# Optimization experiments

Measured on AMD Instinct MI355X. Metric: run time of the kernel, lower is better.

Reference implementation:

```python
import math
import jax, jax.numpy as jnp
import numpy as np

B, S, E, H = 2, 2048, 1024, 16
DK = E // H

def setup_inputs() -> dict:
    key = jax.random.key(0)
    ks = jax.random.split(key, 12)
    sc = 1.0 / math.sqrt(E)
    return {
        "x": jax.random.normal(ks[0], (B, S, E), jnp.float32),
        "kv": jax.random.normal(ks[1], (B, S, E), jnp.float32),
        "mask": jax.random.randint(ks[2], (B, S), 0, 2, jnp.int32),
        "attn_bias": jax.random.normal(ks[3], (B, S, S), jnp.float32),
        "WQ_w": jax.random.normal(ks[4], (E, E), jnp.float32) * sc,
        "WQ_b": jnp.zeros((E,), jnp.float32),
        "WK_w": jax.random.normal(ks[5], (E, E), jnp.float32) * sc,
        "WK_b": jnp.zeros((E,), jnp.float32),
        "WV_w": jax.random.normal(ks[6], (E, E), jnp.float32) * sc,
        "WV_b": jnp.zeros((E,), jnp.float32),
        "WO_w": jax.random.normal(ks[7], (E, E), jnp.float32) * sc,
        "WO_b": jnp.zeros((E,), jnp.float32),
    }

def reference(x, kv, mask, attn_bias, WQ_w, WQ_b, WK_w, WK_b, WV_w, WV_b, WO_w, WO_b):
    b, sq, _ = x.shape
    sk = kv.shape[1]
    # projections, split heads: [B,S,E] -> [B,H,S,DK]
    Q = (x @ WQ_w.T + WQ_b).reshape(b, sq, H, DK).transpose(0, 2, 1, 3)
    K = (kv @ WK_w.T + WK_b).reshape(b, sk, H, DK).transpose(0, 2, 1, 3)
    V = (kv @ WV_w.T + WV_b).reshape(b, sk, H, DK).transpose(0, 2, 1, 3)
    # scores [B,H,Sq,Sk]
    T = jnp.einsum('bhqd,bhkd->bhqk', Q, K) / math.sqrt(DK)
    T = T + attn_bias[:, None, :, :]  # 3D bias broadcast over heads
    m2 = jnp.einsum('bi,bj->bij', mask.astype(T.dtype), mask.astype(T.dtype))
    T = jnp.where(m2[:, None, :, :] == 0, jnp.asarray(-1e9, T.dtype), T)
    A = jax.nn.softmax(T, axis=-1)
    out = jnp.einsum('bhqk,bhkd->bhqd', A, V)  # [B,H,Sq,DK]
    out = out.transpose(0, 2, 1, 3).reshape(b, sq, E)
    return out @ WO_w.T + WO_b
```

## Files before the change

kernel.cpp:

```cpp
#include <hip/hip_runtime.h>

#define DEV static __device__ __forceinline__

typedef __attribute__((ext_vector_type(8))) __bf16 bf16x8;
typedef __attribute__((ext_vector_type(4))) float f32x4;

constexpr int CB = 2;
constexpr int CS = 2048;
constexpr int CE = 1024;
constexpr int CH = 16;
constexpr int CD = 64;
constexpr float LOG2E = 1.44269504f;

DEV unsigned short f2bf(float x) {
  unsigned int u = __float_as_uint(x);
  u += 0x7fffu + ((u >> 16) & 1u);
  return (unsigned short)(u >> 16);
}

DEV f32x4 mfma32(bf16x8 a, bf16x8 b, f32x4 c) {
  return __builtin_amdgcn_mfma_f32_16x16x32_bf16(a, b, c, 0, 0, 0);
}

DEV unsigned int cvtpk(float lo, float hi) {
  unsigned int r;
  asm("v_cvt_pk_bf16_f32 %0, %1, %2" : "=v"(r) : "v"(lo), "v"(hi));
  return r;
}

DEV float exp2r(float x) {
#if __has_builtin(__builtin_amdgcn_exp2f)
  return __builtin_amdgcn_exp2f(x);
#else
  float r; asm("v_exp_f32 %0, %1" : "=v"(r) : "v"(x)); return r;
#endif
}

DEV f32x4 unpk(unsigned int a, unsigned int b) {
  f32x4 r;
  r[0] = __uint_as_float(a << 16);
  r[1] = __uint_as_float(a & 0xffff0000u);
  r[2] = __uint_as_float(b << 16);
  r[3] = __uint_as_float(b & 0xffff0000u);
  return r;
}

DEV void stage16(const void* g, void* l) {
  __builtin_amdgcn_global_load_lds(
      (const __attribute__((address_space(1))) unsigned int*)g,
      (__attribute__((address_space(3))) unsigned int*)l, 16, 0, 0);
}

DEV void cvt_body(long i, const float* __restrict__ x, const float* __restrict__ kv,
                  const float* __restrict__ w0, const float* __restrict__ w1,
                  const float* __restrict__ w2, const float* __restrict__ w3,
                  unsigned short* __restrict__ out) {
  const long NE = (long)CB * CS * CE;
  const long WE = (long)CE * CE;
  const float* src;
  long off = i;
  if (i < NE) {
    src = x;
  } else if (i < 2 * NE) {
    src = kv; off = i - NE;
  } else {
    long j = i - 2 * NE;
    int wi = (int)(j >> 20);
    src = wi == 0 ? w0 : wi == 1 ? w1 : wi == 2 ? w2 : w3;
    off = j & (WE - 1);
  }
  float4 a = *reinterpret_cast<const float4*>(src + off);
  float4 b = *reinterpret_cast<const float4*>(src + off + 4);
  uint4 v;
  v.x = (unsigned int)f2bf(a.x) | ((unsigned int)f2bf(a.y) << 16);
  v.y = (unsigned int)f2bf(a.z) | ((unsigned int)f2bf(a.w) << 16);
  v.z = (unsigned int)f2bf(b.x) | ((unsigned int)f2bf(b.y) << 16);
  v.w = (unsigned int)f2bf(b.z) | ((unsigned int)f2bf(b.w) << 16);
  *reinterpret_cast<uint4*>(out + i) = v;
}

DEV void mbias_body(long idx, const float* __restrict__ bias, const int* __restrict__ mask,
                    unsigned short* __restrict__ mb16) {
  const int b = (int)(idx >> 22);
  const int q = (int)((idx >> 11) & (CS - 1));
  const int k0 = (int)(idx & (CS - 1));
  const bool mq = mask[b * CS + q] != 0;
  const int4 mk0 = *reinterpret_cast<const int4*>(mask + b * CS + k0);
  const int4 mk1 = *reinterpret_cast<const int4*>(mask + b * CS + k0 + 4);
  const float4 b0 = *reinterpret_cast<const float4*>(bias + idx);
  const float4 b1 = *reinterpret_cast<const float4*>(bias + idx + 4);
  const float NEG = -1e9f * LOG2E;
  float v[8];
  if (mq) {
    v[0] = (mk0.x != 0) ? b0.x * LOG2E : NEG;
    v[1] = (mk0.y != 0) ? b0.y * LOG2E : NEG;
    v[2] = (mk0.z != 0) ? b0.z * LOG2E : NEG;
    v[3] = (mk0.w != 0) ? b0.w * LOG2E : NEG;
    v[4] = (mk1.x != 0) ? b1.x * LOG2E : NEG;
    v[5] = (mk1.y != 0) ? b1.y * LOG2E : NEG;
    v[6] = (mk1.z != 0) ? b1.z * LOG2E : NEG;
    v[7] = (mk1.w != 0) ? b1.w * LOG2E : NEG;
  } else {
#pragma unroll
    for (int j = 0; j < 8; j++) v[j] = 0.f;
  }
  uint4 o;
  o.x = cvtpk(v[0], v[1]); o.y = cvtpk(v[2], v[3]);
  o.z = cvtpk(v[4], v[5]); o.w = cvtpk(v[6], v[7]);
  *reinterpret_cast<uint4*>(mb16 + idx) = o;
}

__global__ __launch_bounds__(256) void prep_all(const float* __restrict__ x,
                                                const float* __restrict__ kv,
                                                const float* __restrict__ w0,
                                                const float* __restrict__ w1,
                                                const float* __restrict__ w2,
                                                const float* __restrict__ w3,
                                                unsigned short* __restrict__ outcvt,
                                                const float* __restrict__ bias,
                                                const int* __restrict__ mask,
                                                unsigned short* __restrict__ mb16) {
  const long CVTB = (2 * (long)CB * CS * CE + 4 * (long)CE * CE) / 2048;
  if (blockIdx.x < CVTB) {
    cvt_body(((long)blockIdx.x * 256 + threadIdx.x) * 8, x, kv, w0, w1, w2, w3, outcvt);
  } else {
    mbias_body(((long)(blockIdx.x - CVTB) * 256 + threadIdx.x) * 8, bias, mask, mb16);
  }
}

__global__ __launch_bounds__(256) void cvt_all(const float* __restrict__ x,
                                               const float* __restrict__ kv,
                                               const float* __restrict__ w0,
                                               const float* __restrict__ w1,
                                               const float* __restrict__ w2,
                                               const float* __restrict__ w3,
                                               unsigned short* __restrict__ out) {
  cvt_body(((long)blockIdx.x * 256 + threadIdx.x) * 8, x, kv, w0, w1, w2, w3, out);
}
__global__ __launch_bounds__(256) void mk_mbias(const float* __restrict__ bias,
                                                const int* __restrict__ mask,
                                                unsigned short* __restrict__ mb16) {
  mbias_body(((long)blockIdx.x * 256 + threadIdx.x) * 8, bias, mask, mb16);
}

__global__ __launch_bounds__(256) void gemm_qkv(const unsigned short* __restrict__ xb,
                                                const unsigned short* __restrict__ kvb,
                                                const unsigned short* __restrict__ Wall,
                                                const float* __restrict__ bq,
                                                const float* __restrict__ bk,
                                                const float* __restrict__ bv,
                                                unsigned short* __restrict__ Qb) {
  __shared__ __align__(16) unsigned short As[128 * 64];
  __shared__ __align__(16) unsigned short Bs[128 * 64];
  const long NE = (long)CB * CS * CE;
  const long WE = (long)CE * CE;
  const int which = blockIdx.y >> 3;
  const int n0 = (blockIdx.y & 7) * 128;
  const unsigned short* A = which == 0 ? xb : kvb;
  const unsigned short* W = Wall + (long)which * WE;
  const float* bias = which == 0 ? bq : which == 1 ? bk : bv;
  const int tid = threadIdx.x;
  const int lane = tid & 63, wave = tid >> 6;
  const int wm = (wave >> 1) * 64, wn = (wave & 1) * 64;
  const int g = lane >> 4, rr = lane & 15;
  const int m0 = blockIdx.x * 128;
  const int K = CE;
  f32x4 acc[4][4] = {};

  for (int k0 = 0; k0 < K; k0 += 64) {
#pragma unroll
    for (int t = 0; t < 4; t++) {
      const int u = t * 256 + tid;
      const int row = u >> 3, ce = (u & 7) * 8;
      const int lb = (t * 256 + (tid & 192)) * 16;
      stage16(A + (long)(m0 + row) * K + k0 + ce, (char*)As + lb);
      stage16(W + (long)(n0 + row) * K + k0 + ce, (char*)Bs + lb);
    }
    __syncthreads();
#pragma unroll
    for (int kk = 0; kk < 2; kk++) {
      bf16x8 af[4], bfr[4];
#pragma unroll
      for (int i = 0; i < 4; i++)
        af[i] = *reinterpret_cast<const bf16x8*>(&As[(wm + i * 16 + rr) * 64 + kk * 32 + g * 8]);
#pragma unroll
      for (int j = 0; j < 4; j++)
        bfr[j] = *reinterpret_cast<const bf16x8*>(&Bs[(wn + j * 16 + rr) * 64 + kk * 32 + g * 8]);
#pragma unroll
      for (int i = 0; i < 4; i++)
#pragma unroll
        for (int j = 0; j < 4; j++)
          acc[i][j] = mfma32(af[i], bfr[j], acc[i][j]);
    }
    __syncthreads();
  }

  const float scale = which == 0 ? 0.125f * LOG2E : 1.0f;
#pragma unroll
  for (int i = 0; i < 4; i++) {
#pragma unroll
    for (int j = 0; j < 4; j++) {
      const int colg = n0 + wn + j * 16 + rr;
      const float bvv = bias[colg];
      if (which == 2) {
        const int rowbase = m0 + wm + i * 16 + g * 4;
        const int bb = rowbase >> 11, s = rowbase & 2047;
        const int hh = colg >> 6, d = colg & 63;
        uint2 val;
        val.x = (unsigned int)f2bf(acc[i][j][0] + bvv) | ((unsigned int)f2bf(acc[i][j][1] + bvv) << 16);
        val.y = (unsigned int)f2bf(acc[i][j][2] + bvv) | ((unsigned int)f2bf(acc[i][j][3] + bvv) << 16);
        *reinterpret_cast<uint2*>(Qb + 2 * NE + ((long)((bb * CH + hh) * CD + d)) * CS + s) = val;
      } else {
        unsigned short* outp = Qb + (long)which * NE;
#pragma unroll
        for (int r = 0; r < 4; r++) {
          const int row = m0 + wm + i * 16 + g * 4 + r;
          outp[(long)row * CE + colg] = f2bf((acc[i][j][r] + bvv) * scale);
        }
      }
    }
  }
}

__global__ __launch_bounds__(256) void gemm_wo(const unsigned short* __restrict__ A,
                                               const unsigned short* __restrict__ W,
                                               const float* __restrict__ bias,
                                               float* __restrict__ out) {
  __shared__ __align__(16) unsigned short As[128 * 64];
  __shared__ __align__(16) unsigned short Bs[64 * 64];
  const int tid = threadIdx.x;
  const int lane = tid & 63, wave = tid >> 6;
  const int wm = (wave >> 1) * 64, wn = (wave & 1) * 32;
  const int g = lane >> 4, rr = lane & 15;
  const int m0 = blockIdx.x * 128, n0 = blockIdx.y * 64;
  const int K = CE;
  f32x4 acc[4][2] = {};

  for (int k0 = 0; k0 < K; k0 += 64) {
#pragma unroll
    for (int t = 0; t < 4; t++) {
      const int u = t * 256 + tid;
      const int row = u >> 3, ce = (u & 7) * 8;
      stage16(A + (long)(m0 + row) * K + k0 + ce, (char*)As + (t * 256 + (tid & 192)) * 16);
    }
#pragma unroll
    for (int t = 0; t < 2; t++) {
      const int u = t * 256 + tid;
      const int row = u >> 3, ce = (u & 7) * 8;
      stage16(W + (long)(n0 + row) * K + k0 + ce, (char*)Bs + (t * 256 + (tid & 192)) * 16);
    }
    __syncthreads();
#pragma unroll
    for (int kk = 0; kk < 2; kk++) {
      bf16x8 af[4], bfr[2];
#pragma unroll
      for (int i = 0; i < 4; i++)
        af[i] = *reinterpret_cast<const bf16x8*>(&As[(wm + i * 16 + rr) * 64 + kk * 32 + g * 8]);
#pragma unroll
      for (int j = 0; j < 2; j++)
        bfr[j] = *reinterpret_cast<const bf16x8*>(&Bs[(wn + j * 16 + rr) * 64 + kk * 32 + g * 8]);
#pragma unroll
      for (int i = 0; i < 4; i++)
#pragma unroll
        for (int j = 0; j < 2; j++)
          acc[i][j] = mfma32(af[i], bfr[j], acc[i][j]);
    }
    __syncthreads();
  }

#pragma unroll
  for (int i = 0; i < 4; i++)
#pragma unroll
    for (int j = 0; j < 2; j++) {
      const int colg = n0 + wn + j * 16 + rr;
      const float bvv = bias[colg];
#pragma unroll
      for (int r = 0; r < 4; r++) {
        const int row = m0 + wm + i * 16 + g * 4 + r;
        out[(long)row * CE + colg] = acc[i][j][r] + bvv;
      }
    }
}

__global__ __launch_bounds__(256, 2) void attn_kernel(const unsigned short* __restrict__ Qb,
                                                      const unsigned short* __restrict__ Kb,
                                                      const unsigned short* __restrict__ Vtw,
                                                      const unsigned short* __restrict__ mb16,
                                                      const int* __restrict__ mask,
                                                      unsigned short* __restrict__ AO) {
  __shared__ __align__(16) unsigned char lds[65536];
  const int h = blockIdx.x, qt = blockIdx.y, b = blockIdx.z;
  const int tid = threadIdx.x;
  const int lane = tid & 63, w = tid >> 6;
  const int g = lane >> 4, c = lane & 15;
  const int qbase = qt * 128 + w * 32;

  bf16x8 qf[2][2];
#pragma unroll
  for (int qb = 0; qb < 2; qb++) {
    const unsigned short* Qrow = Qb + ((long)b * CS + qbase + qb * 16 + c) * CE + h * CD;
    qf[qb][0] = *reinterpret_cast<const bf16x8*>(Qrow + g * 8);
    qf[qb][1] = *reinterpret_cast<const bf16x8*>(Qrow + 32 + g * 8);
    if (mask[b * CS + qbase + qb * 16 + c] == 0) {
      qf[qb][0] = bf16x8{}; qf[qb][1] = bf16x8{};
    }
  }

  const unsigned char *kg[4], *vg[4];
  {
    const unsigned char* Ksrc = (const unsigned char*)(Kb + (long)b * CS * CE + h * CD);
    const unsigned char* Vsrc = (const unsigned char*)(Vtw + (long)(b * CH + h) * CD * CS);
    const int rr8 = lane >> 3;
    const int csw = ((lane & 7) << 4) ^ (rr8 << 4);
#pragma unroll
    for (int t = 0; t < 4; t++) {
      const int krow = t * 32 + w * 8 + rr8;
      const int key = (krow & 96) + ((krow >> 2) & 3) * 8 + ((krow >> 4) & 1) * 4 + (krow & 3);
      kg[t] = Ksrc + (long)key * (CE * 2) + csw;
      const int vrow = (t & 1) * 32 + w * 8 + rr8;
      vg[t] = Vsrc + (long)vrow * (CS * 2) + (t >> 1) * 128 + csw;
    }
  }
  const int sw = (c & 7) << 4;
  const unsigned char* rb0 = lds + c * 128 + ((g * 16) ^ sw);
  const unsigned char* rb1 = lds + c * 128 + ((64 + g * 16) ^ sw);

  const unsigned short* mbp0 = mb16 + ((long)b * CS + qbase + c) * CS + g * 8;
  const unsigned short* mbp1 = mb16 + ((long)b * CS + qbase + 16 + c) * CS + g * 8;

  f32x4 o[2][4] = {};
  f32x4 lsum4[2] = {};
  uint4 mbr[2][4];

  auto stage = [&](int bo) {
    unsigned char* kbuf = lds + bo;
    unsigned char* vbuf = lds + bo + 16384;
#pragma unroll
    for (int t = 0; t < 4; t++) {
      stage16(kg[t], kbuf + t * 4096 + w * 1024);
      stage16(vg[t], vbuf + (t >> 1) * 8192 + (t & 1) * 4096 + w * 1024);
      kg[t] += 128 * CE * 2;
      vg[t] += 128 * 2;
    }
  };
  auto load_mb = [&](bool adv) {
#pragma unroll
    for (int kb = 0; kb < 4; kb++) {
      mbr[0][kb] = *reinterpret_cast<const uint4*>(mbp0 + kb * 32);
      mbr[1][kb] = *reinterpret_cast<const uint4*>(mbp1 + kb * 32);
    }
    if (adv) { mbp0 += 128; mbp1 += 128; }
  };

  auto compute = [&](int bo, bool adv) {
    f32x4 sf[2][8];
    __builtin_amdgcn_s_setprio(1);
#pragma unroll
    for (int cb = 0; cb < 8; cb++) {
      const bf16x8 kf0 = *reinterpret_cast<const bf16x8*>(rb0 + bo + cb * 2048);
      const bf16x8 kf1 = *reinterpret_cast<const bf16x8*>(rb1 + bo + cb * 2048);
#pragma unroll
      for (int qb = 0; qb < 2; qb++) {
        const uint4 m = mbr[qb][cb >> 1];
        const f32x4 ci = (cb & 1) ? unpk(m.z, m.w) : unpk(m.x, m.y);
        f32x4 t = mfma32(kf0, qf[qb][0], ci);
        sf[qb][cb] = mfma32(kf1, qf[qb][1], t);
      }
    }
    __builtin_amdgcn_s_setprio(0);
    load_mb(adv);
    uint4 pw[2][4];
#pragma unroll
    for (int qb = 0; qb < 2; qb++)
#pragma unroll
      for (int kb = 0; kb < 4; kb++)
#pragma unroll
        for (int half = 0; half < 2; half++) {
          const int cb = 2 * kb + half;
          f32x4 pv;
          pv[0] = exp2r(sf[qb][cb][0]);
          pv[1] = exp2r(sf[qb][cb][1]);
          pv[2] = exp2r(sf[qb][cb][2]);
          pv[3] = exp2r(sf[qb][cb][3]);
          lsum4[qb] = lsum4[qb] + pv;
          if (half == 0) { pw[qb][kb].x = cvtpk(pv[0], pv[1]); pw[qb][kb].y = cvtpk(pv[2], pv[3]); }
          else           { pw[qb][kb].z = cvtpk(pv[0], pv[1]); pw[qb][kb].w = cvtpk(pv[2], pv[3]); }
        }
    __builtin_amdgcn_s_setprio(1);
#pragma unroll
    for (int nb = 0; nb < 4; nb++) {
#pragma unroll
      for (int kb = 0; kb < 4; kb++) {
        const unsigned char* rbx = (kb & 1) ? rb1 : rb0;
        const bf16x8 vf = *reinterpret_cast<const bf16x8*>(
            rbx + bo + 16384 + (kb >> 1) * 8192 + nb * 2048);
#pragma unroll
        for (int qb = 0; qb < 2; qb++)
          o[qb][nb] = mfma32(vf, __builtin_bit_cast(bf16x8, pw[qb][kb]), o[qb][nb]);
      }
    }
    __builtin_amdgcn_s_setprio(0);
  };

  stage(0);
  load_mb(true);
  stage(32768);

#pragma unroll 1
  for (int it = 0; it < 8; ++it) {
    asm volatile("s_waitcnt vmcnt(16)" ::: "memory");
    __builtin_amdgcn_s_barrier();
    __builtin_amdgcn_sched_barrier(0);
    compute(0, it < 7);
    __builtin_amdgcn_sched_barrier(0);
    __builtin_amdgcn_s_barrier();
    stage(0);
    asm volatile("s_waitcnt vmcnt(16)" ::: "memory");
    __builtin_amdgcn_s_barrier();
    __builtin_amdgcn_sched_barrier(0);
    compute(32768, it < 7);
    __builtin_amdgcn_sched_barrier(0);
    __builtin_amdgcn_s_barrier();
    stage(32768);
  }

#pragma unroll
  for (int qb = 0; qb < 2; qb++) {
    float lsum = (lsum4[qb][0] + lsum4[qb][1]) + (lsum4[qb][2] + lsum4[qb][3]);
    lsum += __shfl_xor(lsum, 16, 64);
    lsum += __shfl_xor(lsum, 32, 64);
    const float linv = 1.0f / lsum;
    unsigned short* Orow = AO + ((long)b * CS + qbase + qb * 16 + c) * CE + h * CD;
#pragma unroll
    for (int nb = 0; nb < 4; nb++) {
      uint2 val;
      val.x = (unsigned int)f2bf(o[qb][nb][0] * linv) | ((unsigned int)f2bf(o[qb][nb][1] * linv) << 16);
      val.y = (unsigned int)f2bf(o[qb][nb][2] * linv) | ((unsigned int)f2bf(o[qb][nb][3] * linv) << 16);
      *reinterpret_cast<uint2*>(Orow + nb * 16 + g * 4) = val;
    }
  }
  asm volatile("s_waitcnt vmcnt(0)" ::: "memory");
}

extern "C" void kernel_launch(void* const* d_in, const int* in_sizes, int n_in,
                              void* d_out, int out_size, void* d_ws, size_t ws_size,
                              hipStream_t stream) {
  (void)in_sizes; (void)n_in; (void)out_size;
  const float* x    = (const float*)d_in[0];
  const float* kv   = (const float*)d_in[1];
  const int*   mask = (const int*)d_in[2];
  const float* ab   = (const float*)d_in[3];
  const float* WQw  = (const float*)d_in[4];
  const float* WQb  = (const float*)d_in[5];
  const float* WKw  = (const float*)d_in[6];
  const float* WKb  = (const float*)d_in[7];
  const float* WVw  = (const float*)d_in[8];
  const float* WVb  = (const float*)d_in[9];
  const float* WOw  = (const float*)d_in[10];
  const float* WOb  = (const float*)d_in[11];
  float* out = (float*)d_out;

  const long NE = (long)CB * CS * CE;
  const long WE = (long)CE * CE;
  unsigned short* ws  = (unsigned short*)d_ws;
  unsigned short* xb  = ws;
  unsigned short* kvb = xb + NE;
  unsigned short* wqb = kvb + NE;
  unsigned short* wob = wqb + 3 * WE;
  unsigned short* Qb  = wob + WE;
  unsigned short* AO  = Qb + 3 * NE;

  const long TOT = 2 * NE + 4 * WE;
  const long MBE = (long)CB * CS * CS;
  const long needShorts = 8 * NE + 4 * WE;
  const bool fused = ws_size >= (size_t)needShorts * 2;

  dim3 ggq(32, 24), gb(256, 1, 1);
  if (fused) {
    unsigned short* mb16 = AO + NE;
    prep_all<<<(int)((TOT + MBE) / 2048), 256, 0, stream>>>(x, kv, WQw, WKw, WVw, WOw, xb,
                                                            ab, mask, mb16);
    gemm_qkv<<<ggq, gb, 0, stream>>>(xb, kvb, wqb, WQb, WKb, WVb, Qb);
    attn_kernel<<<dim3(CH, CS / 128, CB), 256, 0, stream>>>(
        Qb, Qb + NE, Qb + 2 * NE, mb16, mask, AO);
  } else {
    unsigned short* mb16 = xb;
    cvt_all<<<(int)(TOT / 2048), 256, 0, stream>>>(x, kv, WQw, WKw, WVw, WOw, xb);
    gemm_qkv<<<ggq, gb, 0, stream>>>(xb, kvb, wqb, WQb, WKb, WVb, Qb);
    mk_mbias<<<(int)(MBE / 2048), 256, 0, stream>>>(ab, mask, mb16);
    attn_kernel<<<dim3(CH, CS / 128, CB), 256, 0, stream>>>(
        Qb, Qb + NE, Qb + 2 * NE, mb16, mask, AO);
  }

  gemm_wo<<<dim3(32, 16), gb, 0, stream>>>(AO, wob, WOb, out);
}
```

Baseline: 143.1 us.

## Rewrite QKV GEMM with 256x256 tiles, double-buffered LDS and swizzle

The QKV projection GEMM moves from 128x128 tiles with 256 threads to 256x256 tiles with 512 threads (8 waves, 128x64 per wave). Its LDS is now double-buffered with an XOR swizzle, global-to-LDS staging is interleaved with MFMA groups through explicit vmcnt/lgkmcnt waits and barriers, and MFMA sections run at raised priority. The aim is to overlap memory loads with compute and raise data reuse per tile. In exchange the grid drops to 192 blocks, which may underfill the GPU, and the hand-tuned wait counts are fragile.

Result: faster. 136.4 us (-4.7%).

```diff
diff --git a/kernel.cpp b/kernel.cpp
--- a/kernel.cpp
+++ b/kernel.cpp
@@ -143,67 +143,114 @@
   mbias_body(((long)blockIdx.x * 256 + threadIdx.x) * 8, bias, mask, mb16);
 }
 
-__global__ __launch_bounds__(256) void gemm_qkv(const unsigned short* __restrict__ xb,
+__global__ __launch_bounds__(512) void gemm_qkv(const unsigned short* __restrict__ xb,
                                                 const unsigned short* __restrict__ kvb,
                                                 const unsigned short* __restrict__ Wall,
                                                 const float* __restrict__ bq,
                                                 const float* __restrict__ bk,
                                                 const float* __restrict__ bv,
                                                 unsigned short* __restrict__ Qb) {
-  __shared__ __align__(16) unsigned short As[128 * 64];
-  __shared__ __align__(16) unsigned short Bs[128 * 64];
+  __shared__ __align__(16) unsigned char ldsA[32768];
+  __shared__ __align__(16) unsigned char ldsB[32768];
   const long NE = (long)CB * CS * CE;
   const long WE = (long)CE * CE;
-  const int which = blockIdx.y >> 3;
-  const int n0 = (blockIdx.y & 7) * 128;
-  const unsigned short* A = which == 0 ? xb : kvb;
-  const unsigned short* W = Wall + (long)which * WE;
+  const int which = blockIdx.y >> 2;
+  const int n0 = (blockIdx.y & 3) * 256;
+  const int m0 = blockIdx.x * 256;
+  const unsigned char* Ab = (const unsigned char*)(which == 0 ? xb : kvb);
+  const unsigned char* Bb = (const unsigned char*)(Wall + (long)which * WE);
   const float* bias = which == 0 ? bq : which == 1 ? bk : bv;
+
   const int tid = threadIdx.x;
-  const int lane = tid & 63, wave = tid >> 6;
-  const int wm = (wave >> 1) * 64, wn = (wave & 1) * 64;
+  const int lane = tid & 63, w = tid >> 6;
+  const int wr = w >> 2, wc = w & 3;
   const int g = lane >> 4, rr = lane & 15;
-  const int m0 = blockIdx.x * 128;
-  const int K = CE;
-  f32x4 acc[4][4] = {};
-
-  for (int k0 = 0; k0 < K; k0 += 64) {
-#pragma unroll
-    for (int t = 0; t < 4; t++) {
-      const int u = t * 256 + tid;
-      const int row = u >> 3, ce = (u & 7) * 8;
-      const int lb = (t * 256 + (tid & 192)) * 16;
-      stage16(A + (long)(m0 + row) * K + k0 + ce, (char*)As + lb);
-      stage16(W + (long)(n0 + row) * K + k0 + ce, (char*)Bs + lb);
-    }
-    __syncthreads();
-#pragma unroll
-    for (int kk = 0; kk < 2; kk++) {
-      bf16x8 af[4], bfr[4];
-#pragma unroll
-      for (int i = 0; i < 4; i++)
-        af[i] = *reinterpret_cast<const bf16x8*>(&As[(wm + i * 16 + rr) * 64 + kk * 32 + g * 8]);
+
+  const int srow = tid >> 2;
+  const int scsw = ((tid & 3) * 16) ^ (((tid >> 5) & 1) << 5);
+  const unsigned char* apR0 = Ab + ((long)(m0 + srow) * CE) * 2 + scsw;
+  const unsigned char* apR1 = Ab + ((long)(m0 + 128 + srow) * CE) * 2 + scsw;
+  const unsigned char* bpR0 = Bb + ((long)(n0 + srow) * CE) * 2 + scsw;
+  const unsigned char* bpR1 = Bb + ((long)(n0 + 128 + srow) * CE) * 2 + scsw;
+
+  const int cswz = (g * 16) ^ (((rr >> 3) & 1) << 5);
+  const unsigned char* rbA = ldsA + wr * 8192 + rr * 64 + cswz;
+  const unsigned char* rbB = ldsB + wc * 4096 + rr * 64 + cswz;
+
+  f32x4 acc[8][4] = {};
+
+  auto stA = [&](int buf) {
+    stage16(apR0, ldsA + buf * 16384 + w * 1024);
+    stage16(apR1, ldsA + buf * 16384 + 8192 + w * 1024);
+    apR0 += 64; apR1 += 64;
+  };
+  auto stB = [&](int buf) {
+    stage16(bpR0, ldsB + buf * 16384 + w * 1024);
+    stage16(bpR1, ldsB + buf * 16384 + 8192 + w * 1024);
+    bpR0 += 64; bpR1 += 64;
+  };
+
+  stB(0);
+  stA(0);
+  stB(1);
+  asm volatile("s_waitcnt vmcnt(3)" ::: "memory");
+  __builtin_amdgcn_s_barrier();
+
+  auto group = [&](int buf) {
+    bf16x8 ar[4], br[4];
+#pragma unroll
+    for (int ii = 0; ii < 4; ii++)
+      ar[ii] = *reinterpret_cast<const bf16x8*>(rbA + buf * 16384 + ii * 1024);
+#pragma unroll
+    for (int j = 0; j < 4; j++)
+      br[j] = *reinterpret_cast<const bf16x8*>(rbB + buf * 16384 + j * 1024);
+    stA(buf ^ 1);
+    __builtin_amdgcn_s_barrier();
+    asm volatile("s_waitcnt lgkmcnt(0)" ::: "memory");
+    __builtin_amdgcn_sched_barrier(0);
+    __builtin_amdgcn_s_setprio(1);
+#pragma unroll
+    for (int ii = 0; ii < 4; ii++)
 #pragma unroll
       for (int j = 0; j < 4; j++)
-        bfr[j] = *reinterpret_cast<const bf16x8*>(&Bs[(wn + j * 16 + rr) * 64 + kk * 32 + g * 8]);
-#pragma unroll
-      for (int i = 0; i < 4; i++)
-#pragma unroll
-        for (int j = 0; j < 4; j++)
-          acc[i][j] = mfma32(af[i], bfr[j], acc[i][j]);
-    }
-    __syncthreads();
-  }
+        acc[ii][j] = mfma32(ar[ii], br[j], acc[ii][j]);
+    __builtin_amdgcn_s_setprio(0);
+    asm volatile("s_waitcnt vmcnt(4)" ::: "memory");
+    __builtin_amdgcn_s_barrier();
+#pragma unroll
+    for (int ii = 0; ii < 4; ii++)
+      ar[ii] = *reinterpret_cast<const bf16x8*>(rbA + buf * 16384 + 4096 + ii * 1024);
+    stB(buf);
+    __builtin_amdgcn_s_barrier();
+    asm volatile("s_waitcnt lgkmcnt(0)" ::: "memory");
+    __builtin_amdgcn_sched_barrier(0);
+    __builtin_amdgcn_s_setprio(1);
+#pragma unroll
+    for (int ii = 0; ii < 4; ii++)
+#pragma unroll
+      for (int j = 0; j < 4; j++)
+        acc[4 + ii][j] = mfma32(ar[ii], br[j], acc[4 + ii][j]);
+    __builtin_amdgcn_s_setprio(0);
+    asm volatile("s_waitcnt vmcnt(3)" ::: "memory");
+    __builtin_amdgcn_s_barrier();
+  };
+
+#pragma unroll 1
+  for (int it = 0; it < 16; ++it) {
+    group(0);
+    group(1);
+  }
+  asm volatile("s_waitcnt vmcnt(0)" ::: "memory");
 
   const float scale = which == 0 ? 0.125f * LOG2E : 1.0f;
 #pragma unroll
-  for (int i = 0; i < 4; i++) {
+  for (int i = 0; i < 8; i++) {
 #pragma unroll
     for (int j = 0; j < 4; j++) {
-      const int colg = n0 + wn + j * 16 + rr;
+      const int colg = n0 + wc * 64 + j * 16 + rr;
       const float bvv = bias[colg];
       if (which == 2) {
-        const int rowbase = m0 + wm + i * 16 + g * 4;
+        const int rowbase = m0 + wr * 128 + i * 16 + g * 4;
         const int bb = rowbase >> 11, s = rowbase & 2047;
         const int hh = colg >> 6, d = colg & 63;
         uint2 val;
@@ -214,7 +261,7 @@
         unsigned short* outp = Qb + (long)which * NE;
 #pragma unroll
         for (int r = 0; r < 4; r++) {
-          const int row = m0 + wm + i * 16 + g * 4 + r;
+          const int row = m0 + wr * 128 + i * 16 + g * 4 + r;
           outp[(long)row * CE + colg] = f2bf((acc[i][j][r] + bvv) * scale);
         }
       }
@@ -475,22 +522,21 @@
   const long needShorts = 8 * NE + 4 * WE;
   const bool fused = ws_size >= (size_t)needShorts * 2;
 
-  dim3 ggq(32, 24), gb(256, 1, 1);
   if (fused) {
     unsigned short* mb16 = AO + NE;
     prep_all<<<(int)((TOT + MBE) / 2048), 256, 0, stream>>>(x, kv, WQw, WKw, WVw, WOw, xb,
                                                             ab, mask, mb16);
-    gemm_qkv<<<ggq, gb, 0, stream>>>(xb, kvb, wqb, WQb, WKb, WVb, Qb);
+    gemm_qkv<<<dim3(16, 12), 512, 0, stream>>>(xb, kvb, wqb, WQb, WKb, WVb, Qb);
     attn_kernel<<<dim3(CH, CS / 128, CB), 256, 0, stream>>>(
         Qb, Qb + NE, Qb + 2 * NE, mb16, mask, AO);
   } else {
     unsigned short* mb16 = xb;
     cvt_all<<<(int)(TOT / 2048), 256, 0, stream>>>(x, kv, WQw, WKw, WVw, WOw, xb);
-    gemm_qkv<<<ggq, gb, 0, stream>>>(xb, kvb, wqb, WQb, WKb, WVb, Qb);
+    gemm_qkv<<<dim3(16, 12), 512, 0, stream>>>(xb, kvb, wqb, WQb, WKb, WVb, Qb);
     mk_mbias<<<(int)(MBE / 2048), 256, 0, stream>>>(ab, mask, mb16);
     attn_kernel<<<dim3(CH, CS / 128, CB), 256, 0, stream>>>(
         Qb, Qb + NE, Qb + 2 * NE, mb16, mask, AO);
   }
 
-  gemm_wo<<<dim3(32, 16), gb, 0, stream>>>(AO, wob, WOb, out);
-}
+  gemm_wo<<<dim3(32, 16), 256, 0, stream>>>(AO, wob, WOb, out);
+}
```
